# Kernel tuning notes

Hardware: AMD Instinct MI355X
Metric: run time of the kernel (lower is better)

The kernel has to match this reference:

```python
import jax, jax.numpy as jnp
import numpy as np
import math

C = 16
K = 16
M = 64
DEPTH = 4          # int(sqrt(K)) tree depth
D = C * 9          # input feature dim, 9 dims per codebook subspace
N = 1024 * 128     # rows
N_NODES = K - 1    # 15 internal nodes of a depth-4 binary tree


def _selection_matrix(C):
    # node i at tree level l reads the per-codebook hashed feature at depth index l
    S = np.zeros((C * N_NODES, C * DEPTH), np.float32)
    for c in range(C):
        for i in range(N_NODES):
            level = 0 if i == 0 else (1 if i < 3 else (2 if i < 7 else 3))
            S[c * N_NODES + i, c * DEPTH + level] = 1.0
    return S


def _bit_matrix(C, K):
    # row (c,k): +/-1 on the 4 tree nodes along code k's root-to-leaf path;
    # matching code scores DEPTH, every other code scores <= DEPTH-2
    B = np.zeros((C * K, C * N_NODES), np.float32)
    for c in range(C):
        for k in range(K):
            prefix = 0
            for l in range(DEPTH):
                bit = (k >> (DEPTH - 1 - l)) & 1
                node = (2 ** l - 1) + prefix
                B[c * K + k, c * N_NODES + node] = 1.0 if bit else -1.0
                prefix = prefix * 2 + bit
    return B


def setup_inputs() -> dict:
    key = jax.random.key(0)
    k1, k2, k3, k4 = jax.random.split(key, 4)
    I = jax.random.normal(k1, (N, D), jnp.float32) - 0.5
    A = jax.random.normal(k2, (C, D // C, DEPTH), jnp.float32)   # soft hashing projections
    T = jax.random.normal(k3, (C * N_NODES,), jnp.float32)       # node thresholds
    bound = math.sqrt(1.0 / (C * K))  # kaiming_uniform with a=sqrt(5), fan_in=C*K
    L = jax.random.uniform(k4, (M, C, K), jnp.float32, -bound, bound)  # lookup tables
    S = jnp.asarray(_selection_matrix(C))
    B = jnp.asarray(_bit_matrix(C, K))
    return {"I": I, "A": A, "T": T, "L": L, "S": S, "B": B}


def reference(I, A, T, L, S, B):
    n = I.shape[0]
    # per-codebook soft hash: (n, C, D//C) x (C, D//C, DEPTH) -> (n, C*DEPTH)
    h = jnp.einsum('ncd,cdp->ncp', I.reshape(n, C, D // C), A).reshape(n, C * DEPTH)
    # thresholded tree decisions with straight-through sign
    b = h @ S.T - T                                   # (n, C*15)
    t = jnp.tanh(b)
    s = jax.lax.stop_gradient(jnp.sign(b) - t) + t    # fwd: sign, bwd: tanh'
    # bit-matrix decode of path agreements -> per-code scores
    scores = (s @ B.T).reshape(n, C, K)               # (n, C, K), max DEPTH at true code
    onehot = jax.nn.one_hot(jnp.argmax(scores, axis=2), K, dtype=I.dtype)
    E = jax.lax.stop_gradient(onehot - scores) + scores  # STE one-hot encoding
    # LUT gather-accumulate: out[n,m] = sum_c L[m,c,code(n,c)]
    return jnp.einsum('nck,mck->nm', E, L)
```

## Files before the change

kernel.cpp:

```cpp
#include <hip/hip_runtime.h>
#include <hip/hip_fp16.h>


#define NROWS (1024 * 128)

__global__ __launch_bounds__(256, 2) void halut_fwd(
    const float* __restrict__ I,
    const float* __restrict__ A,
    const float* __restrict__ T,
    const float* __restrict__ L,
    float* __restrict__ out)
{
    __shared__ uint32_t sBuf[8192];
    __shared__ double   sA[576];
    __shared__ double   sT[256];

    const int tid = threadIdx.x;

    {
        uint4* lut4 = (uint4*)sBuf;
        #pragma unroll
        for (int q = 0; q < 8; ++q) {
            uint32_t w[4];
            #pragma unroll
            for (int e = 0; e < 4; ++e) {
                const float fa = L[(8 * q + 2 * e)     * 256 + tid];
                const float fb = L[(8 * q + 2 * e + 1) * 256 + tid];
                w[e] = ((uint32_t)__half_as_ushort(__float2half_rn(fb)) << 16)
                     |  (uint32_t)__half_as_ushort(__float2half_rn(fa));
            }
            lut4[q * 256 + tid] = make_uint4(w[0], w[1], w[2], w[3]);
        }
    }
    for (int i = tid; i < 576; i += 256) sA[i] = (double)A[i];
    {
        const int c = tid >> 4, j = tid & 15;
        sT[tid] = (j < 15) ? (double)T[c * 15 + j] : 0.0;
    }
    __syncthreads();

    const int row = blockIdx.x * 256 + tid;
    const float* rp = I + (size_t)row * 144;

    __half2 acc2[32];
    #pragma unroll
    for (int k = 0; k < 32; ++k) acc2[k] = __floats2half2_rn(0.f, 0.f);

    const uint4* lut4 = (const uint4*)sBuf;

    float4 bufA[9], bufB[9];
    #pragma unroll
    for (int i = 0; i < 9; ++i) bufA[i] = ((const float4*)rp)[i];

    #pragma unroll
    for (int g = 0; g < 4; ++g) {
        const float* curp = (const float*)((g & 1) ? bufB : bufA);
        if (g < 3) {
            float4* nxt = (g & 1) ? bufA : bufB;
            const float4* src = (const float4*)(rp + (g + 1) * 36);
            #pragma unroll
            for (int i = 0; i < 9; ++i) nxt[i] = src[i];
        }
        #pragma unroll
        for (int cc = 0; cc < 4; ++cc) {
            const int c = g * 4 + cc;
            double h0 = 0.0, h1 = 0.0, h2 = 0.0, h3 = 0.0;
            #pragma unroll
            for (int d = 0; d < 9; ++d) {
                const double  x   = (double)curp[cc * 9 + d];
                const double2 a01 = *(const double2*)&sA[(c * 9 + d) * 4];
                const double2 a23 = *(const double2*)&sA[(c * 9 + d) * 4 + 2];
                h0 = fma(x, a01.x, h0);
                h1 = fma(x, a01.y, h1);
                h2 = fma(x, a23.x, h2);
                h3 = fma(x, a23.y, h3);
            }
            const double2* tp = (const double2*)&sT[c * 16];
            const double2 t0 = tp[0], t1 = tp[1], t2 = tp[2], t3 = tp[3];
            const double2 t4 = tp[4], t5 = tp[5], t6 = tp[6], t7 = tp[7];
            uint32_t mk = 0;
            mk |= (h0 > t0.x) ?     1u : 0u;
            mk |= (h1 > t0.y) ?     2u : 0u;
            mk |= (h1 > t1.x) ?     4u : 0u;
            mk |= (h2 > t1.y) ?     8u : 0u;
            mk |= (h2 > t2.x) ?    16u : 0u;
            mk |= (h2 > t2.y) ?    32u : 0u;
            mk |= (h2 > t3.x) ?    64u : 0u;
            mk |= (h3 > t3.y) ?   128u : 0u;
            mk |= (h3 > t4.x) ?   256u : 0u;
            mk |= (h3 > t4.y) ?   512u : 0u;
            mk |= (h3 > t5.x) ?  1024u : 0u;
            mk |= (h3 > t5.y) ?  2048u : 0u;
            mk |= (h3 > t6.x) ?  4096u : 0u;
            mk |= (h3 > t6.y) ?  8192u : 0u;
            mk |= (h3 > t7.x) ? 16384u : 0u;
            int p =       (int)(mk & 1u);
            p = 2 * p + (int)((mk >> (1 + p)) & 1u);
            p = 2 * p + (int)((mk >> (3 + p)) & 1u);
            p = 2 * p + (int)((mk >> (7 + p)) & 1u);

            const uint4* colp = lut4 + (c << 4) + p;
            #pragma unroll
            for (int q = 0; q < 8; ++q) {
                const uint4 w = colp[q << 8];
                acc2[q * 4 + 0] = __hadd2(acc2[q * 4 + 0], *(const __half2*)&w.x);
                acc2[q * 4 + 1] = __hadd2(acc2[q * 4 + 1], *(const __half2*)&w.y);
                acc2[q * 4 + 2] = __hadd2(acc2[q * 4 + 2], *(const __half2*)&w.z);
                acc2[q * 4 + 3] = __hadd2(acc2[q * 4 + 3], *(const __half2*)&w.w);
            }
        }
    }

    __syncthreads();
    float* sO = (float*)sBuf;
    #pragma unroll
    for (int half = 0; half < 2; ++half) {
        if ((tid >> 7) == half) {
            const int r = tid & 127;
            #pragma unroll
            for (int ch = 0; ch < 16; ++ch) {
                const float4 v = make_float4(__low2float (acc2[2 * ch]),
                                             __high2float(acc2[2 * ch]),
                                             __low2float (acc2[2 * ch + 1]),
                                             __high2float(acc2[2 * ch + 1]));
                *(float4*)&sO[(r << 6) + ((ch ^ (r & 15)) << 2)] = v;
            }
        }
        __syncthreads();
        float4* op = (float4*)(out + (size_t)blockIdx.x * (256 * 64)
                                   + (size_t)half * (128 * 64));
        #pragma unroll
        for (int j = 0; j < 8; ++j) {
            const int F  = tid + (j << 8);
            const int r2 = F >> 4;
            const int m2 = F & 15;
            op[F] = *(const float4*)&sO[(r2 << 6) + ((m2 ^ (r2 & 15)) << 2)];
        }
        __syncthreads();
    }
}

extern "C" void kernel_launch(void* const* d_in, const int* in_sizes, int n_in,
                              void* d_out, int out_size, void* d_ws, size_t ws_size,
                              hipStream_t stream) {
    const float* I = (const float*)d_in[0];
    const float* A = (const float*)d_in[1];
    const float* T = (const float*)d_in[2];
    const float* L = (const float*)d_in[3];
    float* outp = (float*)d_out;

    const int nblocks = NROWS / 256;
    halut_fwd<<<nblocks, 256, 0, stream>>>(I, A, T, L, outp);
}
```

Measured before the change: 30.51 us.

## Move A/T to global double workspace via prep kernel, drop double-buffered loads

```diff
diff --git a/kernel.cpp b/kernel.cpp
--- a/kernel.cpp
+++ b/kernel.cpp
@@ -4,16 +4,23 @@
 
 #define NROWS (1024 * 128)
 
-__global__ __launch_bounds__(256, 2) void halut_fwd(
-    const float* __restrict__ I,
+__global__ __launch_bounds__(1024) void halut_prep(
     const float* __restrict__ A,
     const float* __restrict__ T,
+    double* __restrict__ W)
+{
+    const int t = threadIdx.x;
+    if (t < 576) W[t] = (double)A[t];
+    if (t >= 576 && t < 816) W[t] = (double)T[t - 576];
+}
+
+__global__ __launch_bounds__(256, 4) void halut_fwd(
+    const float* __restrict__ I,
+    const double* __restrict__ W,
     const float* __restrict__ L,
     float* __restrict__ out)
 {
     __shared__ uint32_t sBuf[8192];
-    __shared__ double   sA[576];
-    __shared__ double   sT[256];
 
     const int tid = threadIdx.x;
 
@@ -32,12 +39,10 @@
             lut4[q * 256 + tid] = make_uint4(w[0], w[1], w[2], w[3]);
         }
     }
-    for (int i = tid; i < 576; i += 256) sA[i] = (double)A[i];
-    {
-        const int c = tid >> 4, j = tid & 15;
-        sT[tid] = (j < 15) ? (double)T[c * 15 + j] : 0.0;
-    }
     __syncthreads();
+
+    const double* __restrict__ Aw = W;
+    const double* __restrict__ Tw = W + 576;
 
     const int row = blockIdx.x * 256 + tid;
     const float* rp = I + (size_t)row * 144;
@@ -48,52 +53,46 @@
 
     const uint4* lut4 = (const uint4*)sBuf;
 
-    float4 bufA[9], bufB[9];
-    #pragma unroll
-    for (int i = 0; i < 9; ++i) bufA[i] = ((const float4*)rp)[i];
-
     #pragma unroll
     for (int g = 0; g < 4; ++g) {
-        const float* curp = (const float*)((g & 1) ? bufB : bufA);
-        if (g < 3) {
-            float4* nxt = (g & 1) ? bufA : bufB;
-            const float4* src = (const float4*)(rp + (g + 1) * 36);
+        float4 buf[9];
+        {
+            const float4* rv = (const float4*)(rp + g * 36);
             #pragma unroll
-            for (int i = 0; i < 9; ++i) nxt[i] = src[i];
+            for (int i = 0; i < 9; ++i) buf[i] = rv[i];
         }
+        const float* bf = (const float*)buf;
+
         #pragma unroll
         for (int cc = 0; cc < 4; ++cc) {
             const int c = g * 4 + cc;
             double h0 = 0.0, h1 = 0.0, h2 = 0.0, h3 = 0.0;
             #pragma unroll
             for (int d = 0; d < 9; ++d) {
-                const double  x   = (double)curp[cc * 9 + d];
-                const double2 a01 = *(const double2*)&sA[(c * 9 + d) * 4];
-                const double2 a23 = *(const double2*)&sA[(c * 9 + d) * 4 + 2];
-                h0 = fma(x, a01.x, h0);
-                h1 = fma(x, a01.y, h1);
-                h2 = fma(x, a23.x, h2);
-                h3 = fma(x, a23.y, h3);
+                const double x = (double)bf[cc * 9 + d];
+                const int    b = (c * 9 + d) * 4;
+                h0 = fma(x, Aw[b + 0], h0);
+                h1 = fma(x, Aw[b + 1], h1);
+                h2 = fma(x, Aw[b + 2], h2);
+                h3 = fma(x, Aw[b + 3], h3);
             }
-            const double2* tp = (const double2*)&sT[c * 16];
-            const double2 t0 = tp[0], t1 = tp[1], t2 = tp[2], t3 = tp[3];
-            const double2 t4 = tp[4], t5 = tp[5], t6 = tp[6], t7 = tp[7];
+            const double* tp = Tw + c * 15;
             uint32_t mk = 0;
-            mk |= (h0 > t0.x) ?     1u : 0u;
-            mk |= (h1 > t0.y) ?     2u : 0u;
-            mk |= (h1 > t1.x) ?     4u : 0u;
-            mk |= (h2 > t1.y) ?     8u : 0u;
-            mk |= (h2 > t2.x) ?    16u : 0u;
-            mk |= (h2 > t2.y) ?    32u : 0u;
-            mk |= (h2 > t3.x) ?    64u : 0u;
-            mk |= (h3 > t3.y) ?   128u : 0u;
-            mk |= (h3 > t4.x) ?   256u : 0u;
-            mk |= (h3 > t4.y) ?   512u : 0u;
-            mk |= (h3 > t5.x) ?  1024u : 0u;
-            mk |= (h3 > t5.y) ?  2048u : 0u;
-            mk |= (h3 > t6.x) ?  4096u : 0u;
-            mk |= (h3 > t6.y) ?  8192u : 0u;
-            mk |= (h3 > t7.x) ? 16384u : 0u;
+            mk |= (h0 > tp[0])  ?     1u : 0u;
+            mk |= (h1 > tp[1])  ?     2u : 0u;
+            mk |= (h1 > tp[2])  ?     4u : 0u;
+            mk |= (h2 > tp[3])  ?     8u : 0u;
+            mk |= (h2 > tp[4])  ?    16u : 0u;
+            mk |= (h2 > tp[5])  ?    32u : 0u;
+            mk |= (h2 > tp[6])  ?    64u : 0u;
+            mk |= (h3 > tp[7])  ?   128u : 0u;
+            mk |= (h3 > tp[8])  ?   256u : 0u;
+            mk |= (h3 > tp[9])  ?   512u : 0u;
+            mk |= (h3 > tp[10]) ?  1024u : 0u;
+            mk |= (h3 > tp[11]) ?  2048u : 0u;
+            mk |= (h3 > tp[12]) ?  4096u : 0u;
+            mk |= (h3 > tp[13]) ?  8192u : 0u;
+            mk |= (h3 > tp[14]) ? 16384u : 0u;
             int p =       (int)(mk & 1u);
             p = 2 * p + (int)((mk >> (1 + p)) & 1u);
             p = 2 * p + (int)((mk >> (3 + p)) & 1u);
@@ -148,7 +147,9 @@
     const float* T = (const float*)d_in[2];
     const float* L = (const float*)d_in[3];
     float* outp = (float*)d_out;
+    double* W = (double*)d_ws;
 
+    halut_prep<<<1, 1024, 0, stream>>>(A, T, W);
     const int nblocks = NROWS / 256;
-    halut_fwd<<<nblocks, 256, 0, stream>>>(I, A, T, L, outp);
+    halut_fwd<<<nblocks, 256, 0, stream>>>(I, W, L, outp);
 }
```

Measured after the change: 43.37 us. 42.2% more time.

## Stage input rows through LDS with coalesced loads and per-codebook lane mapping

Applied to the files above, without the earlier changes.

```diff
diff --git a/kernel.cpp b/kernel.cpp
--- a/kernel.cpp
+++ b/kernel.cpp
@@ -11,108 +11,126 @@
     const float* __restrict__ L,
     float* __restrict__ out)
 {
-    __shared__ uint32_t sBuf[8192];
-    __shared__ double   sA[576];
-    __shared__ double   sT[256];
+    __shared__ uint32_t sLut[8192];
+    __shared__ float    sStage[4][2304];
+    __shared__ uint8_t  sCodes[4096];
 
-    const int tid = threadIdx.x;
+    const int tid  = threadIdx.x;
+    const int w    = tid >> 6;
+    const int lane = tid & 63;
+
+    const int cB = lane & 15;
+    const int g  = lane >> 4;
+    float Af[36];
+    {
+        const float4* ap4 = (const float4*)(A + cB * 36);
+        #pragma unroll
+        for (int i = 0; i < 9; ++i) {
+            const float4 v = ap4[i];
+            Af[4*i+0] = v.x; Af[4*i+1] = v.y; Af[4*i+2] = v.z; Af[4*i+3] = v.w;
+        }
+    }
+    float Tf[15];
+    #pragma unroll
+    for (int j = 0; j < 15; ++j) Tf[j] = T[cB * 15 + j];
 
     {
-        uint4* lut4 = (uint4*)sBuf;
+        uint4* lut4 = (uint4*)sLut;
         #pragma unroll
         for (int q = 0; q < 8; ++q) {
-            uint32_t w[4];
+            uint32_t wv[4];
             #pragma unroll
             for (int e = 0; e < 4; ++e) {
-                const float fa = L[(8 * q + 2 * e)     * 256 + tid];
-                const float fb = L[(8 * q + 2 * e + 1) * 256 + tid];
-                w[e] = ((uint32_t)__half_as_ushort(__float2half_rn(fb)) << 16)
-                     |  (uint32_t)__half_as_ushort(__float2half_rn(fa));
+                const float fa = L[(8*q + 2*e)     * 256 + tid];
+                const float fb = L[(8*q + 2*e + 1) * 256 + tid];
+                wv[e] = ((uint32_t)__half_as_ushort(__float2half_rn(fb)) << 16)
+                      |  (uint32_t)__half_as_ushort(__float2half_rn(fa));
             }
-            lut4[q * 256 + tid] = make_uint4(w[0], w[1], w[2], w[3]);
+            lut4[q * 256 + tid] = make_uint4(wv[0], wv[1], wv[2], wv[3]);
         }
-    }
-    for (int i = tid; i < 576; i += 256) sA[i] = (double)A[i];
-    {
-        const int c = tid >> 4, j = tid & 15;
-        sT[tid] = (j < 15) ? (double)T[c * 15 + j] : 0.0;
     }
     __syncthreads();
 
-    const int row = blockIdx.x * 256 + tid;
-    const float* rp = I + (size_t)row * 144;
+    const int wave_row0 = blockIdx.x * 256 + w * 64;
+    const float4* Isrc = (const float4*)I;
+    float4* st4 = (float4*)sStage[w];
+
+    float4 nbuf[9];
+    #pragma unroll
+    for (int i = 0; i < 9; ++i)
+        nbuf[i] = Isrc[(size_t)wave_row0 * 36 + i * 64 + lane];
+
+    #pragma unroll
+    for (int p16 = 0; p16 < 4; ++p16) {
+        #pragma unroll
+        for (int i = 0; i < 9; ++i) st4[i * 64 + lane] = nbuf[i];
+        if (p16 < 3) {
+            #pragma unroll
+            for (int i = 0; i < 9; ++i)
+                nbuf[i] = Isrc[(size_t)(wave_row0 + (p16+1)*16) * 36 + i*64 + lane];
+        }
+        #pragma unroll
+        for (int ps = 0; ps < 4; ++ps) {
+            const int lr = ps * 4 + g;
+            const float* xr = &sStage[w][lr * 144 + cB * 9];
+            double h0 = 0.0, h1 = 0.0, h2 = 0.0, h3 = 0.0;
+            #pragma unroll
+            for (int d = 0; d < 9; ++d) {
+                const double x = (double)xr[d];
+                h0 = fma(x, (double)Af[4*d+0], h0);
+                h1 = fma(x, (double)Af[4*d+1], h1);
+                h2 = fma(x, (double)Af[4*d+2], h2);
+                h3 = fma(x, (double)Af[4*d+3], h3);
+            }
+            uint32_t mk = 0;
+            mk |= (h0 > (double)Tf[0])  ?     1u : 0u;
+            mk |= (h1 > (double)Tf[1])  ?     2u : 0u;
+            mk |= (h1 > (double)Tf[2])  ?     4u : 0u;
+            mk |= (h2 > (double)Tf[3])  ?     8u : 0u;
+            mk |= (h2 > (double)Tf[4])  ?    16u : 0u;
+            mk |= (h2 > (double)Tf[5])  ?    32u : 0u;
+            mk |= (h2 > (double)Tf[6])  ?    64u : 0u;
+            mk |= (h3 > (double)Tf[7])  ?   128u : 0u;
+            mk |= (h3 > (double)Tf[8])  ?   256u : 0u;
+            mk |= (h3 > (double)Tf[9])  ?   512u : 0u;
+            mk |= (h3 > (double)Tf[10]) ?  1024u : 0u;
+            mk |= (h3 > (double)Tf[11]) ?  2048u : 0u;
+            mk |= (h3 > (double)Tf[12]) ?  4096u : 0u;
+            mk |= (h3 > (double)Tf[13]) ?  8192u : 0u;
+            mk |= (h3 > (double)Tf[14]) ? 16384u : 0u;
+            int p =       (int)(mk & 1u);
+            p = 2 * p + (int)((mk >> (1 + p)) & 1u);
+            p = 2 * p + (int)((mk >> (3 + p)) & 1u);
+            p = 2 * p + (int)((mk >> (7 + p)) & 1u);
+            sCodes[(w * 64 + p16 * 16 + lr) * 16 + cB] = (uint8_t)p;
+        }
+    }
+
+    const uint4 cw = *(const uint4*)&sCodes[tid * 16];
+    const uint32_t cd0 = cw.x, cd1 = cw.y, cd2 = cw.z, cd3 = cw.w;
 
     __half2 acc2[32];
     #pragma unroll
     for (int k = 0; k < 32; ++k) acc2[k] = __floats2half2_rn(0.f, 0.f);
 
-    const uint4* lut4 = (const uint4*)sBuf;
-
-    float4 bufA[9], bufB[9];
-    #pragma unroll
-    for (int i = 0; i < 9; ++i) bufA[i] = ((const float4*)rp)[i];
-
-    #pragma unroll
-    for (int g = 0; g < 4; ++g) {
-        const float* curp = (const float*)((g & 1) ? bufB : bufA);
-        if (g < 3) {
-            float4* nxt = (g & 1) ? bufA : bufB;
-            const float4* src = (const float4*)(rp + (g + 1) * 36);
-            #pragma unroll
-            for (int i = 0; i < 9; ++i) nxt[i] = src[i];
-        }
+    const uint4* lut4 = (const uint4*)sLut;
+    #pragma unroll 4
+    for (int c = 0; c < 16; ++c) {
+        const uint32_t cdw = (c < 4) ? cd0 : (c < 8) ? cd1 : (c < 12) ? cd2 : cd3;
+        const int p = (int)((cdw >> ((c & 3) * 8)) & 15u);
+        const uint4* colp = lut4 + (c << 4) + p;
         #pragma unroll
-        for (int cc = 0; cc < 4; ++cc) {
-            const int c = g * 4 + cc;
-            double h0 = 0.0, h1 = 0.0, h2 = 0.0, h3 = 0.0;
-            #pragma unroll
-            for (int d = 0; d < 9; ++d) {
-                const double  x   = (double)curp[cc * 9 + d];
-                const double2 a01 = *(const double2*)&sA[(c * 9 + d) * 4];
-                const double2 a23 = *(const double2*)&sA[(c * 9 + d) * 4 + 2];
-                h0 = fma(x, a01.x, h0);
-                h1 = fma(x, a01.y, h1);
-                h2 = fma(x, a23.x, h2);
-                h3 = fma(x, a23.y, h3);
-            }
-            const double2* tp = (const double2*)&sT[c * 16];
-            const double2 t0 = tp[0], t1 = tp[1], t2 = tp[2], t3 = tp[3];
-            const double2 t4 = tp[4], t5 = tp[5], t6 = tp[6], t7 = tp[7];
-            uint32_t mk = 0;
-            mk |= (h0 > t0.x) ?     1u : 0u;
-            mk |= (h1 > t0.y) ?     2u : 0u;
-            mk |= (h1 > t1.x) ?     4u : 0u;
-            mk |= (h2 > t1.y) ?     8u : 0u;
-            mk |= (h2 > t2.x) ?    16u : 0u;
-            mk |= (h2 > t2.y) ?    32u : 0u;
-            mk |= (h2 > t3.x) ?    64u : 0u;
-            mk |= (h3 > t3.y) ?   128u : 0u;
-            mk |= (h3 > t4.x) ?   256u : 0u;
-            mk |= (h3 > t4.y) ?   512u : 0u;
-            mk |= (h3 > t5.x) ?  1024u : 0u;
-            mk |= (h3 > t5.y) ?  2048u : 0u;
-            mk |= (h3 > t6.x) ?  4096u : 0u;
-            mk |= (h3 > t6.y) ?  8192u : 0u;
-            mk |= (h3 > t7.x) ? 16384u : 0u;
-            int p =       (int)(mk & 1u);
-            p = 2 * p + (int)((mk >> (1 + p)) & 1u);
-            p = 2 * p + (int)((mk >> (3 + p)) & 1u);
-            p = 2 * p + (int)((mk >> (7 + p)) & 1u);
-
-            const uint4* colp = lut4 + (c << 4) + p;
-            #pragma unroll
-            for (int q = 0; q < 8; ++q) {
-                const uint4 w = colp[q << 8];
-                acc2[q * 4 + 0] = __hadd2(acc2[q * 4 + 0], *(const __half2*)&w.x);
-                acc2[q * 4 + 1] = __hadd2(acc2[q * 4 + 1], *(const __half2*)&w.y);
-                acc2[q * 4 + 2] = __hadd2(acc2[q * 4 + 2], *(const __half2*)&w.z);
-                acc2[q * 4 + 3] = __hadd2(acc2[q * 4 + 3], *(const __half2*)&w.w);
-            }
+        for (int q = 0; q < 8; ++q) {
+            const uint4 wv = colp[q << 8];
+            acc2[q*4+0] = __hadd2(acc2[q*4+0], *(const __half2*)&wv.x);
+            acc2[q*4+1] = __hadd2(acc2[q*4+1], *(const __half2*)&wv.y);
+            acc2[q*4+2] = __hadd2(acc2[q*4+2], *(const __half2*)&wv.z);
+            acc2[q*4+3] = __hadd2(acc2[q*4+3], *(const __half2*)&wv.w);
         }
     }
 
     __syncthreads();
-    float* sO = (float*)sBuf;
+    float* sO = (float*)sLut;
     #pragma unroll
     for (int half = 0; half < 2; ++half) {
         if ((tid >> 7) == half) {
```

Result: faster. 27.26 us, median of 2 (-10.6%).
